# Optimization experiments

Measured on AMD Instinct MI355X. Metric: run time of the kernel, lower is better.

The kernel has to match this reference:

```python
import jax, jax.numpy as jnp
import numpy as np

H = W = 20
NVARS = 4          # n_predictor_vars
NK = 12            # n_conv2d_kernels
NF = NK + NVARS + 1  # 17 augmented channels (conv + original + time)
SIGLEN = NF + NF * NF  # 306, depth-2 signature length
T_END = 1.0        # self.T in the module


def setup_inputs() -> dict:
    key = jax.random.key(0)
    ks = jax.random.split(key, 8)
    B, T = 64, 96
    x = jax.random.normal(ks[0], (B, T, NVARS, H, W), dtype=jnp.float32)
    conv_w = jax.random.normal(ks[1], (NK, NVARS, 3, 3), dtype=jnp.float32) * 0.1
    conv_b = jax.random.normal(ks[2], (NK,), dtype=jnp.float32) * 0.01
    d_in = SIGLEN * H * W  # 122400

    def lin(k, fan_in, fan_out):
        return jax.random.normal(k, (fan_in, fan_out), dtype=jnp.float32) / np.float32(np.sqrt(fan_in))

    w1, b1 = lin(ks[3], d_in, 32), jnp.zeros((32,), jnp.float32)
    w2, b2 = lin(ks[4], 32, 32), jnp.zeros((32,), jnp.float32)
    w3, b3 = lin(ks[5], 32, 32), jnp.zeros((32,), jnp.float32)
    w4, b4 = lin(ks[6], 32, 1), jnp.zeros((1,), jnp.float32)
    return {"x": x, "conv_w": conv_w, "conv_b": conv_b,
            "w1": w1, "b1": b1, "w2": w2, "b2": b2,
            "w3": w3, "b3": b3, "w4": w4, "b4": b4}


def reference(x, conv_w, conv_b, w1, b1, w2, b2, w3, b3, w4, b4):
    B, T = x.shape[0], x.shape[1]
    # Batched conv over all timesteps at once (the torch code loops over t).
    xi = x.reshape(B * T, NVARS, H, W)
    y = jax.lax.conv_general_dilated(
        xi, conv_w, window_strides=(1, 1), padding='SAME',
        dimension_numbers=('NCHW', 'OIHW', 'NCHW'))
    y = y + conv_b[None, :, None, None]
    y = y.reshape(B, T, NK, H, W)
    # Dropout3d is identity in eval mode.
    # Augment: [conv features, original values, time channel] along channel dim.
    tch = jnp.linspace(0.0, T_END, T, dtype=x.dtype).reshape(1, T, 1, 1, 1)
    tch = jnp.broadcast_to(tch, (B, T, 1, H, W))
    feat = jnp.concatenate([y, x, tch], axis=2)        # (B, T, NF, H, W)
    path = jnp.transpose(feat, (0, 3, 4, 1, 2))        # (B, H, W, T, NF)
    # Depth-2 path signature (Chen closed form):
    # level1 = sum dx; level2 = sum_{i<j} dx_i (x) dx_j + 0.5 sum_i dx_i (x) dx_i
    dx = path[..., 1:, :] - path[..., :-1, :]          # (B,H,W,T-1,NF)
    csum = jnp.cumsum(dx, axis=-2)                     # inclusive prefix sums
    lvl1 = csum[..., -1, :]                            # (B,H,W,NF)
    # (exclusive prefix) + 0.5*dx = csum - 0.5*dx -> single contracted einsum
    lvl2 = jnp.einsum('bhwti,bhwtj->bhwij', csum - 0.5 * dx, dx)
    sig = jnp.concatenate([lvl1, lvl2.reshape(B, H, W, NF * NF)], axis=-1)  # (B,H,W,306)
    flat = sig.reshape(B, H * W * SIGLEN)
    h = jax.nn.relu(flat @ w1 + b1)
    h = jax.nn.relu(h @ w2 + b2)
    h = jax.nn.relu(h @ w3 + b3)
    return h @ w4 + b4                                 # (B, 1)
```

## Files before the change

### kernel.cpp

```cpp
#include <hip/hip_runtime.h>

#define HH 20
#define WW 20
#define TT 96
#define BB 64
#define SIG 306
#define NFC 17
#define TSTRIDE 260
#define CHUNK 16
#define NCHUNK 6
#define XT 199
#define KTOT 122400
#define KSLAB 120
#define NSLAB 2
#define NKBLK 510
#define LDT 66

typedef float float4u __attribute__((ext_vector_type(4), aligned(4)));

__global__ __launch_bounds__(256) void sig_kernel(
    const float* __restrict__ x,
    const float* __restrict__ cw,
    float* __restrict__ sig)
{
  __shared__ __align__(16) float feat[15 * TSTRIDE + 256 + 8];
  __shared__ __align__(16) float xs[CHUNK * XT];

  const int tid = threadIdx.x;
  const int blk = blockIdx.x;
  const int b = blk / 25;
  const int tile = blk % 25;
  const int th4 = (tile / 5) * 4, tw4 = (tile % 5) * 4;
  const float* xb0 = x + (size_t)b * TT * 1600;

  int g_off[9], l_off[9];
  #pragma unroll
  for (int r = 0; r < 9; r++) {
    int idx = r * 256 + tid;
    int t = idx / 144, q = idx % 144;
    int ci = q / 36, pos = q % 36, row = pos / 6, col = pos % 6;
    int gr = th4 - 1 + row, gc = tw4 - 1 + col;
    bool valid = (gr >= 0 && gr < HH && gc >= 0 && gc < WW);
    g_off[r] = valid ? (t * 1600 + ci * 400 + gr * WW + gc) : -1;
    l_off[r] = t * XT + ci * 48 + row * 8 + col;
  }

  const int cpix = tid >> 4, ctt = tid & 15;
  const int cpy = cpix >> 2, cpx = cpix & 3;

  const int p2 = tid >> 4;
  const int rr = tid & 15, it = rr >> 2, jt = rr & 3;
  const int i0 = it * 4, j0 = jt * 4;

  float accv[4][4];
  float f0a[4], f0b[4], pa[4], pb[4], fsum[4];
  float rg[9];
  #pragma unroll
  for (int i = 0; i < 4; i++) {
    #pragma unroll
    for (int j = 0; j < 4; j++) accv[i][j] = 0.f;
  }

  auto loadrg = [&](int chunk) {
    const float* xbc = xb0 + (size_t)chunk * CHUNK * 1600;
    #pragma unroll
    for (int r = 0; r < 9; r++)
      rg[r] = (g_off[r] >= 0) ? xbc[g_off[r]] : 0.f;
  };
  auto writexs = [&]() {
    #pragma unroll
    for (int r = 0; r < 9; r++) xs[l_off[r]] = rg[r];
  };

  auto conv = [&]() {
    float win[4][9];
    const int wb2 = ctt * XT;
    #pragma unroll
    for (int ci = 0; ci < 4; ci++)
      #pragma unroll
      for (int dy = 0; dy < 3; dy++)
        #pragma unroll
        for (int dxx = 0; dxx < 3; dxx++)
          win[ci][dy * 3 + dxx] = xs[wb2 + ci * 48 + (cpy + dy) * 8 + (cpx + dxx)];

    float fk[12];
    #pragma unroll
    for (int k = 0; k < 12; k++) {
      float a = 0.f;
      #pragma unroll
      for (int ci = 0; ci < 4; ci++) {
        #pragma unroll
        for (int p = 0; p < 9; p++)
          a += win[ci][p] * cw[k * 36 + ci * 9 + p];
      }
      fk[k] = a;
    }
    float* fr = &feat[ctt * TSTRIDE + cpix * 16];
    *reinterpret_cast<float4*>(fr + 0)  = make_float4(fk[0], fk[1], fk[2], fk[3]);
    *reinterpret_cast<float4*>(fr + 4)  = make_float4(fk[4], fk[5], fk[6], fk[7]);
    *reinterpret_cast<float4*>(fr + 8)  = make_float4(fk[8], fk[9], fk[10], fk[11]);
    *reinterpret_cast<float4*>(fr + 12) = make_float4(win[0][4], win[1][4], win[2][4], win[3][4]);
  };

  auto p2step = [&](int tt) {
    const float* row = &feat[tt * TSTRIDE + p2 * 16];
    const float4 a4 = *reinterpret_cast<const float4*>(row + i0);
    const float4 b4 = *reinterpret_cast<const float4*>(row + j0);
    float fa[4] = {a4.x, a4.y, a4.z, a4.w};
    float fb[4] = {b4.x, b4.y, b4.z, b4.w};
    float sa[4], db[4];
    #pragma unroll
    for (int i = 0; i < 4; i++) { sa[i] = fa[i] + pa[i]; db[i] = fb[i] - pb[i]; }
    #pragma unroll
    for (int i = 0; i < 4; i++)
      #pragma unroll
      for (int j = 0; j < 4; j++) accv[i][j] += sa[i] * db[j];
    #pragma unroll
    for (int i = 0; i < 4; i++) { fsum[i] += fa[i]; pa[i] = fa[i]; pb[i] = fb[i]; }
  };

  loadrg(0);
  writexs();
  __syncthreads();
  conv();
  loadrg(1);
  __syncthreads();
  {
    const float* r0 = &feat[p2 * 16];
    const float4 a4 = *reinterpret_cast<const float4*>(r0 + i0);
    const float4 b4 = *reinterpret_cast<const float4*>(r0 + j0);
    f0a[0] = a4.x; f0a[1] = a4.y; f0a[2] = a4.z; f0a[3] = a4.w;
    f0b[0] = b4.x; f0b[1] = b4.y; f0b[2] = b4.z; f0b[3] = b4.w;
    #pragma unroll
    for (int i = 0; i < 4; i++) { pa[i] = f0a[i]; pb[i] = f0b[i]; fsum[i] = f0a[i]; }
  }
  #pragma unroll
  for (int tt = 1; tt < CHUNK; tt++) p2step(tt);

  for (int chunk = 1; chunk < NCHUNK; chunk++) {
    writexs();
    __syncthreads();
    conv();
    if (chunk < NCHUNK - 1) loadrg(chunk + 1);
    __syncthreads();
    #pragma unroll
    for (int tt = 0; tt < CHUNK; tt++) p2step(tt);
  }

  {
    const int ph = th4 + (p2 >> 2), pw = tw4 + (p2 & 3);
    float* sb = sig + (size_t)b * KTOT + (size_t)(ph * WW + pw) * SIG;
    float lv1b[4];
    #pragma unroll
    for (int j = 0; j < 4; j++) lv1b[j] = pb[j] - f0b[j];
    #pragma unroll
    for (int ii = 0; ii < 4; ii++) {
      float4u v;
      #pragma unroll
      for (int jj = 0; jj < 4; jj++)
        v[jj] = 0.5f * accv[ii][jj] - f0a[ii] * lv1b[jj];
      *reinterpret_cast<float4u*>(sb + NFC + (i0 + ii) * NFC + j0) = v;
    }
    if (jt == 0) {
      #pragma unroll
      for (int ii = 0; ii < 4; ii++) {
        const int c = i0 + ii;
        const float f0 = f0a[ii], f95 = pa[ii], fs = fsum[ii];
        sb[c] = f95 - f0;
        sb[NFC + c * NFC + 16] = (fs - 95.5f * f0 - 0.5f * f95) * (1.f / 95.f);
        sb[NFC + 16 * NFC + c] = (95.5f * f95 + 0.5f * f0 - fs) * (1.f / 95.f);
      }
      if (it == 0) { sb[16] = 1.0f; sb[NFC + 16 * NFC + 16] = 0.5f; }
    }
  }
}

template<bool ATOMIC>
__global__ __launch_bounds__(256) void mlp1_gemm(
    const float* __restrict__ sig, const float* __restrict__ w1,
    float* __restrict__ part)
{
  __shared__ __align__(16) float ldsT[KSLAB * LDT];
  __shared__ __align__(16) float wls[KSLAB * 32];
  const int tid = threadIdx.x;
  const int n = tid & 31, bq = tid >> 5;
  const int k0 = blockIdx.x * (KSLAB * NSLAB);

  float a8[8];
  #pragma unroll
  for (int i = 0; i < 8; i++) a8[i] = 0.f;

  float rA[30], rW[15];
  auto loadslab = [&](int s) {
    const int ks = k0 + s * KSLAB;
    #pragma unroll
    for (int r = 0; r < 30; r++) {
      int idx = r * 256 + tid;
      int b = idx / KSLAB, kk = idx % KSLAB;
      rA[r] = sig[(size_t)b * KTOT + ks + kk];
    }
    #pragma unroll
    for (int r = 0; r < 15; r++)
      rW[r] = w1[(size_t)ks * 32 + r * 256 + tid];
  };

  loadslab(0);
  for (int s = 0; s < NSLAB; s++) {
    if (s) __syncthreads();
    #pragma unroll
    for (int r = 0; r < 30; r++) {
      int idx = r * 256 + tid;
      int b = idx / KSLAB, kk = idx % KSLAB;
      ldsT[kk * LDT + b] = rA[r];
    }
    #pragma unroll
    for (int r = 0; r < 15; r++)
      wls[r * 256 + tid] = rW[r];
    __syncthreads();
    if (s + 1 < NSLAB) loadslab(s + 1);

    #pragma unroll 4
    for (int kk = 0; kk < KSLAB; kk++) {
      const float w = wls[kk * 32 + n];
      const float4 s0 = *reinterpret_cast<const float4*>(&ldsT[kk * LDT + bq * 8]);
      const float4 s1 = *reinterpret_cast<const float4*>(&ldsT[kk * LDT + bq * 8 + 4]);
      a8[0] += s0.x * w; a8[1] += s0.y * w; a8[2] += s0.z * w; a8[3] += s0.w * w;
      a8[4] += s1.x * w; a8[5] += s1.y * w; a8[6] += s1.z * w; a8[7] += s1.w * w;
    }
  }

  if (ATOMIC) {
    #pragma unroll
    for (int i = 0; i < 8; i++)
      atomicAdd(&part[(bq * 8 + i) * 32 + n], a8[i]);
  } else {
    const size_t pb = (size_t)blockIdx.x * (BB * 32);
    #pragma unroll
    for (int i = 0; i < 8; i++)
      part[pb + (bq * 8 + i) * 32 + n] = a8[i];
  }
}

__global__ __launch_bounds__(256) void mlp_tail(
    const float* __restrict__ part, int npart, const float* __restrict__ b1,
    const float* __restrict__ w2, const float* __restrict__ b2,
    const float* __restrict__ w3, const float* __restrict__ b3,
    const float* __restrict__ w4, const float* __restrict__ b4,
    float* __restrict__ out)
{
  __shared__ float red[8][33];
  const int tid = threadIdx.x;
  const int n = tid & 31;
  const int s = tid >> 5;
  const int b = blockIdx.x;

  float sum = 0.f;
  #pragma unroll 8
  for (int p = s; p < npart; p += 8)
    sum += part[(size_t)p * (BB * 32) + b * 32 + n];
  red[s][n] = sum;
  __syncthreads();

  if (tid < 32) {
    float acc = red[0][n];
    #pragma unroll
    for (int q = 1; q < 8; q++) acc += red[q][n];

    float h = fmaxf(acc + b1[n], 0.f);

    float v = b2[n];
    #pragma unroll
    for (int k = 0; k < 32; k++)
      v += __shfl(h, k, 64) * w2[k * 32 + n];
    h = fmaxf(v, 0.f);

    v = b3[n];
    #pragma unroll
    for (int k = 0; k < 32; k++)
      v += __shfl(h, k, 64) * w3[k * 32 + n];
    h = fmaxf(v, 0.f);

    float p = h * w4[n];
    #pragma unroll
    for (int o = 16; o >= 1; o >>= 1) p += __shfl_xor(p, o, 64);
    if (n == 0) out[b] = p + b4[0];
  }
}

extern "C" void kernel_launch(void* const* d_in, const int* in_sizes, int n_in,
                              void* d_out, int out_size, void* d_ws, size_t ws_size,
                              hipStream_t stream) {
  const float* x  = (const float*)d_in[0];
  const float* cw = (const float*)d_in[1];
  const float* w1 = (const float*)d_in[3];
  const float* b1 = (const float*)d_in[4];
  const float* w2 = (const float*)d_in[5];
  const float* b2 = (const float*)d_in[6];
  const float* w3 = (const float*)d_in[7];
  const float* b3 = (const float*)d_in[8];
  const float* w4 = (const float*)d_in[9];
  const float* b4 = (const float*)d_in[10];
  float* out = (float*)d_out;

  const size_t sig_bytes  = (size_t)BB * KTOT * sizeof(float);
  const size_t part_bytes = (size_t)NKBLK * BB * 32 * sizeof(float);
  float* sigm = (float*)d_ws;

  sig_kernel<<<dim3(1600), dim3(256), 0, stream>>>(x, cw, sigm);

  if (ws_size >= sig_bytes + part_bytes) {
    float* part = (float*)((char*)d_ws + sig_bytes);
    mlp1_gemm<false><<<dim3(NKBLK), dim3(256), 0, stream>>>(sigm, w1, part);
    mlp_tail<<<dim3(64), dim3(256), 0, stream>>>(part, NKBLK, b1, w2, b2, w3, b3, w4, b4, out);
  } else {
    float* acc = (float*)((char*)d_ws + sig_bytes);
    hipMemsetAsync(acc, 0, BB * 32 * sizeof(float), stream);
    mlp1_gemm<true><<<dim3(NKBLK), dim3(256), 0, stream>>>(sigm, w1, acc);
    mlp_tail<<<dim3(64), dim3(256), 0, stream>>>(acc, 1, b1, w2, b2, w3, b3, w4, b4, out);
  }
}
```

Measured before the change: 224.0 us.

## Add single-slab first-layer GEMM kernel with more blocks and partials

```diff
diff --git a/kernel.cpp b/kernel.cpp
--- a/kernel.cpp
+++ b/kernel.cpp
@@ -14,6 +14,8 @@
 #define KSLAB 120
 #define NSLAB 2
 #define NKBLK 510
+#define KS2 120
+#define NB2 1020
 #define LDT 66
 
 typedef float float4u __attribute__((ext_vector_type(4), aligned(4)));
@@ -173,6 +175,50 @@
       if (it == 0) { sb[16] = 1.0f; sb[NFC + 16 * NFC + 16] = 0.5f; }
     }
   }
+}
+
+__global__ __launch_bounds__(256) void mlp1_v2(
+    const float* __restrict__ sig, const float* __restrict__ w1,
+    float* __restrict__ part)
+{
+  __shared__ __align__(16) float ldsT[KS2 * LDT];
+  const int tid = threadIdx.x;
+  const int n = tid & 31, bq = tid >> 5;
+  const int ks = blockIdx.x * KS2;
+
+  float rA[30];
+  #pragma unroll
+  for (int r = 0; r < 30; r++) {
+    int idx = r * 256 + tid;
+    int b = idx / KS2, kk = idx % KS2;
+    rA[r] = sig[(size_t)b * KTOT + ks + kk];
+  }
+  #pragma unroll
+  for (int r = 0; r < 30; r++) {
+    int idx = r * 256 + tid;
+    int b = idx / KS2, kk = idx % KS2;
+    ldsT[kk * LDT + b] = rA[r];
+  }
+  __syncthreads();
+
+  float a8[8];
+  #pragma unroll
+  for (int i = 0; i < 8; i++) a8[i] = 0.f;
+
+  const float* wp = w1 + (size_t)ks * 32 + n;
+  #pragma unroll 4
+  for (int kk = 0; kk < KS2; kk++) {
+    const float w = wp[kk * 32];
+    const float4 s0 = *reinterpret_cast<const float4*>(&ldsT[kk * LDT + bq * 8]);
+    const float4 s1 = *reinterpret_cast<const float4*>(&ldsT[kk * LDT + bq * 8 + 4]);
+    a8[0] += s0.x * w; a8[1] += s0.y * w; a8[2] += s0.z * w; a8[3] += s0.w * w;
+    a8[4] += s1.x * w; a8[5] += s1.y * w; a8[6] += s1.z * w; a8[7] += s1.w * w;
+  }
+
+  const size_t pb = (size_t)blockIdx.x * (BB * 32);
+  #pragma unroll
+  for (int i = 0; i < 8; i++)
+    part[pb + (bq * 8 + i) * 32 + n] = a8[i];
 }
 
 template<bool ATOMIC>
@@ -302,13 +348,18 @@
   const float* b4 = (const float*)d_in[10];
   float* out = (float*)d_out;
 
-  const size_t sig_bytes  = (size_t)BB * KTOT * sizeof(float);
-  const size_t part_bytes = (size_t)NKBLK * BB * 32 * sizeof(float);
+  const size_t sig_bytes   = (size_t)BB * KTOT * sizeof(float);
+  const size_t part2_bytes = (size_t)NB2 * BB * 32 * sizeof(float);
+  const size_t part_bytes  = (size_t)NKBLK * BB * 32 * sizeof(float);
   float* sigm = (float*)d_ws;
 
   sig_kernel<<<dim3(1600), dim3(256), 0, stream>>>(x, cw, sigm);
 
-  if (ws_size >= sig_bytes + part_bytes) {
+  if (ws_size >= sig_bytes + part2_bytes) {
+    float* part = (float*)((char*)d_ws + sig_bytes);
+    mlp1_v2<<<dim3(NB2), dim3(256), 0, stream>>>(sigm, w1, part);
+    mlp_tail<<<dim3(64), dim3(256), 0, stream>>>(part, NB2, b1, w2, b2, w3, b3, w4, b4, out);
+  } else if (ws_size >= sig_bytes + part_bytes) {
     float* part = (float*)((char*)d_ws + sig_bytes);
     mlp1_gemm<false><<<dim3(NKBLK), dim3(256), 0, stream>>>(sigm, w1, part);
     mlp_tail<<<dim3(64), dim3(256), 0, stream>>>(part, NKBLK, b1, w2, b2, w3, b3, w4, b4, out);
```

Measured after the change: 226.1 us. Within noise of the previous version (+1.0%).

## Fuse signature computation with first MLP layer, dropping the signature round-trip

Applied to the files above, without the earlier changes.

```diff
diff --git a/kernel.cpp b/kernel.cpp
--- a/kernel.cpp
+++ b/kernel.cpp
@@ -10,26 +10,25 @@
 #define CHUNK 16
 #define NCHUNK 6
 #define XT 199
-#define KTOT 122400
-#define KSLAB 120
-#define NSLAB 2
-#define NKBLK 510
-#define LDT 66
+#define NTILE 25
+#define REDA 4608
 
 typedef float float4u __attribute__((ext_vector_type(4), aligned(4)));
 
-__global__ __launch_bounds__(256) void sig_kernel(
+template<bool ATOMIC>
+__global__ __launch_bounds__(256) void sig_mlp1(
     const float* __restrict__ x,
     const float* __restrict__ cw,
-    float* __restrict__ sig)
+    const float* __restrict__ w1,
+    float* __restrict__ part)
 {
-  __shared__ __align__(16) float feat[15 * TSTRIDE + 256 + 8];
+  __shared__ __align__(16) float feat[REDA];
   __shared__ __align__(16) float xs[CHUNK * XT];
 
   const int tid = threadIdx.x;
-  const int blk = blockIdx.x;
-  const int b = blk / 25;
-  const int tile = blk % 25;
+  const int L = (blockIdx.x & 7) * 200 + (blockIdx.x >> 3);
+  const int tile = L >> 6;
+  const int b = L & 63;
   const int th4 = (tile / 5) * 4, tw4 = (tile % 5) * 4;
   const float* xb0 = x + (size_t)b * TT * 1600;
 
@@ -149,95 +148,104 @@
 
   {
     const int ph = th4 + (p2 >> 2), pw = tw4 + (p2 & 3);
-    float* sb = sig + (size_t)b * KTOT + (size_t)(ph * WW + pw) * SIG;
+    const int pixbase = (ph * WW + pw) * SIG;
     float lv1b[4];
     #pragma unroll
     for (int j = 0; j < 4; j++) lv1b[j] = pb[j] - f0b[j];
-    #pragma unroll
-    for (int ii = 0; ii < 4; ii++) {
-      float4u v;
-      #pragma unroll
-      for (int jj = 0; jj < 4; jj++)
-        v[jj] = 0.5f * accv[ii][jj] - f0a[ii] * lv1b[jj];
-      *reinterpret_cast<float4u*>(sb + NFC + (i0 + ii) * NFC + j0) = v;
+
+    float spv[4]; int spr[4]; int nsp = 0;
+    if (jt == 0) {
+      nsp = 4;
+      #pragma unroll
+      for (int ii = 0; ii < 4; ii++) { spv[ii] = pa[ii] - f0a[ii]; spr[ii] = pixbase + i0 + ii; }
+    } else if (jt == 1) {
+      nsp = 4;
+      #pragma unroll
+      for (int ii = 0; ii < 4; ii++) {
+        spv[ii] = (fsum[ii] - 95.5f * f0a[ii] - 0.5f * pa[ii]) * (1.f / 95.f);
+        spr[ii] = pixbase + NFC + (i0 + ii) * NFC + 16;
+      }
+    } else if (jt == 2) {
+      nsp = 4;
+      #pragma unroll
+      for (int ii = 0; ii < 4; ii++) {
+        spv[ii] = (95.5f * pa[ii] + 0.5f * f0a[ii] - fsum[ii]) * (1.f / 95.f);
+        spr[ii] = pixbase + NFC + 16 * NFC + (i0 + ii);
+      }
+    } else {
+      if (it == 0) { nsp = 1; spv[0] = 1.0f; spr[0] = pixbase + 16; }
+      if (it == 1) { nsp = 1; spv[0] = 0.5f; spr[0] = pixbase + NFC + 16 * NFC + 16; }
     }
-    if (jt == 0) {
+
+    float hs0 = 0.f, hs1 = 0.f;
+    #pragma unroll
+    for (int half = 0; half < 2; half++) {
+      const int n0 = half * 16;
+      float h[16];
+      #pragma unroll
+      for (int q = 0; q < 16; q++) h[q] = 0.f;
+
       #pragma unroll
       for (int ii = 0; ii < 4; ii++) {
-        const int c = i0 + ii;
-        const float f0 = f0a[ii], f95 = pa[ii], fs = fsum[ii];
-        sb[c] = f95 - f0;
-        sb[NFC + c * NFC + 16] = (fs - 95.5f * f0 - 0.5f * f95) * (1.f / 95.f);
-        sb[NFC + 16 * NFC + c] = (95.5f * f95 + 0.5f * f0 - fs) * (1.f / 95.f);
-      }
-      if (it == 0) { sb[16] = 1.0f; sb[NFC + 16 * NFC + 16] = 0.5f; }
+        #pragma unroll
+        for (int jj = 0; jj < 4; jj++) {
+          const float val = 0.5f * accv[ii][jj] - f0a[ii] * lv1b[jj];
+          const float* wr = w1 + (size_t)(pixbase + NFC + (i0 + ii) * NFC + (j0 + jj)) * 32 + n0;
+          const float4 wa = *reinterpret_cast<const float4*>(wr);
+          const float4 wb = *reinterpret_cast<const float4*>(wr + 4);
+          const float4 wc = *reinterpret_cast<const float4*>(wr + 8);
+          const float4 wd = *reinterpret_cast<const float4*>(wr + 12);
+          h[0]  += val * wa.x; h[1]  += val * wa.y; h[2]  += val * wa.z; h[3]  += val * wa.w;
+          h[4]  += val * wb.x; h[5]  += val * wb.y; h[6]  += val * wb.z; h[7]  += val * wb.w;
+          h[8]  += val * wc.x; h[9]  += val * wc.y; h[10] += val * wc.z; h[11] += val * wc.w;
+          h[12] += val * wd.x; h[13] += val * wd.y; h[14] += val * wd.z; h[15] += val * wd.w;
+        }
+      }
+      #pragma unroll
+      for (int sp = 0; sp < 4; sp++) {
+        if (sp < nsp) {
+          const float val = spv[sp];
+          const float* wr = w1 + (size_t)spr[sp] * 32 + n0;
+          const float4 wa = *reinterpret_cast<const float4*>(wr);
+          const float4 wb = *reinterpret_cast<const float4*>(wr + 4);
+          const float4 wc = *reinterpret_cast<const float4*>(wr + 8);
+          const float4 wd = *reinterpret_cast<const float4*>(wr + 12);
+          h[0]  += val * wa.x; h[1]  += val * wa.y; h[2]  += val * wa.z; h[3]  += val * wa.w;
+          h[4]  += val * wb.x; h[5]  += val * wb.y; h[6]  += val * wb.z; h[7]  += val * wb.w;
+          h[8]  += val * wc.x; h[9]  += val * wc.y; h[10] += val * wc.z; h[11] += val * wc.w;
+          h[12] += val * wd.x; h[13] += val * wd.y; h[14] += val * wd.z; h[15] += val * wd.w;
+        }
+      }
+
+      __syncthreads();
+      #pragma unroll
+      for (int q = 0; q < 16; q++) feat[tid * 17 + q] = h[q];
+      __syncthreads();
+      {
+        const int r0 = tid >> 4, nn = tid & 15;
+        float s = 0.f;
+        #pragma unroll
+        for (int j2 = 0; j2 < 16; j2++) s += feat[(r0 + 16 * j2) * 17 + nn];
+        feat[256 * 17 + tid] = s;
+      }
+      __syncthreads();
+      if (tid < 16) {
+        float s = 0.f;
+        #pragma unroll
+        for (int r = 0; r < 16; r++) s += feat[256 * 17 + r * 16 + tid];
+        if (half == 0) hs0 = s; else hs1 = s;
+      }
     }
-  }
-}
-
-template<bool ATOMIC>
-__global__ __launch_bounds__(256) void mlp1_gemm(
-    const float* __restrict__ sig, const float* __restrict__ w1,
-    float* __restrict__ part)
-{
-  __shared__ __align__(16) float ldsT[KSLAB * LDT];
-  __shared__ __align__(16) float wls[KSLAB * 32];
-  const int tid = threadIdx.x;
-  const int n = tid & 31, bq = tid >> 5;
-  const int k0 = blockIdx.x * (KSLAB * NSLAB);
-
-  float a8[8];
-  #pragma unroll
-  for (int i = 0; i < 8; i++) a8[i] = 0.f;
-
-  float rA[30], rW[15];
-  auto loadslab = [&](int s) {
-    const int ks = k0 + s * KSLAB;
-    #pragma unroll
-    for (int r = 0; r < 30; r++) {
-      int idx = r * 256 + tid;
-      int b = idx / KSLAB, kk = idx % KSLAB;
-      rA[r] = sig[(size_t)b * KTOT + ks + kk];
+
+    if (tid < 16) {
+      if (ATOMIC) {
+        atomicAdd(&part[b * 32 + tid], hs0);
+        atomicAdd(&part[b * 32 + 16 + tid], hs1);
+      } else {
+        part[tile * (BB * 32) + b * 32 + tid] = hs0;
+        part[tile * (BB * 32) + b * 32 + 16 + tid] = hs1;
+      }
     }
-    #pragma unroll
-    for (int r = 0; r < 15; r++)
-      rW[r] = w1[(size_t)ks * 32 + r * 256 + tid];
-  };
-
-  loadslab(0);
-  for (int s = 0; s < NSLAB; s++) {
-    if (s) __syncthreads();
-    #pragma unroll
-    for (int r = 0; r < 30; r++) {
-      int idx = r * 256 + tid;
-      int b = idx / KSLAB, kk = idx % KSLAB;
-      ldsT[kk * LDT + b] = rA[r];
-    }
-    #pragma unroll
-    for (int r = 0; r < 15; r++)
-      wls[r * 256 + tid] = rW[r];
-    __syncthreads();
-    if (s + 1 < NSLAB) loadslab(s + 1);
-
-    #pragma unroll 4
-    for (int kk = 0; kk < KSLAB; kk++) {
-      const float w = wls[kk * 32 + n];
-      const float4 s0 = *reinterpret_cast<const float4*>(&ldsT[kk * LDT + bq * 8]);
-      const float4 s1 = *reinterpret_cast<const float4*>(&ldsT[kk * LDT + bq * 8 + 4]);
-      a8[0] += s0.x * w; a8[1] += s0.y * w; a8[2] += s0.z * w; a8[3] += s0.w * w;
-      a8[4] += s1.x * w; a8[5] += s1.y * w; a8[6] += s1.z * w; a8[7] += s1.w * w;
-    }
-  }
-
-  if (ATOMIC) {
-    #pragma unroll
-    for (int i = 0; i < 8; i++)
-      atomicAdd(&part[(bq * 8 + i) * 32 + n], a8[i]);
-  } else {
-    const size_t pb = (size_t)blockIdx.x * (BB * 32);
-    #pragma unroll
-    for (int i = 0; i < 8; i++)
-      part[pb + (bq * 8 + i) * 32 + n] = a8[i];
   }
 }
 
@@ -255,7 +263,6 @@
   const int b = blockIdx.x;
 
   float sum = 0.f;
-  #pragma unroll 8
   for (int p = s; p < npart; p += 8)
     sum += part[(size_t)p * (BB * 32) + b * 32 + n];
   red[s][n] = sum;
@@ -302,20 +309,16 @@
   const float* b4 = (const float*)d_in[10];
   float* out = (float*)d_out;
 
-  const size_t sig_bytes  = (size_t)BB * KTOT * sizeof(float);
-  const size_t part_bytes = (size_t)NKBLK * BB * 32 * sizeof(float);
-  float* sigm = (float*)d_ws;
-
-  sig_kernel<<<dim3(1600), dim3(256), 0, stream>>>(x, cw, sigm);
-
-  if (ws_size >= sig_bytes + part_bytes) {
-    float* part = (float*)((char*)d_ws + sig_bytes);
-    mlp1_gemm<false><<<dim3(NKBLK), dim3(256), 0, stream>>>(sigm, w1, part);
-    mlp_tail<<<dim3(64), dim3(256), 0, stream>>>(part, NKBLK, b1, w2, b2, w3, b3, w4, b4, out);
+  const size_t part_bytes = (size_t)NTILE * BB * 32 * sizeof(float);
+
+  if (ws_size >= part_bytes) {
+    float* part = (float*)d_ws;
+    sig_mlp1<false><<<dim3(1600), dim3(256), 0, stream>>>(x, cw, w1, part);
+    mlp_tail<<<dim3(64), dim3(256), 0, stream>>>(part, NTILE, b1, w2, b2, w3, b3, w4, b4, out);
   } else {
-    float* acc = (float*)((char*)d_ws + sig_bytes);
+    float* acc = (float*)d_ws;
     hipMemsetAsync(acc, 0, BB * 32 * sizeof(float), stream);
-    mlp1_gemm<true><<<dim3(NKBLK), dim3(256), 0, stream>>>(sigm, w1, acc);
+    sig_mlp1<true><<<dim3(1600), dim3(256), 0, stream>>>(x, cw, w1, acc);
     mlp_tail<<<dim3(64), dim3(256), 0, stream>>>(acc, 1, b1, w2, b2, w3, b3, w4, b4, out);
   }
 }
```

Measured after the change: 380.4 us. 1.7x slower.
